# Optimization experiments

Hardware: AMD Instinct MI355X
Metric: run time of the kernel (lower is better)

## Reference

```python
import jax, jax.numpy as jnp
import numpy as np

B, N, F_IN = 8, 4096, 100  # F_IN = num_traj * classification_steps
D = 64                     # node_dim
OUT = 1                    # clasf_out_dim


def setup_inputs() -> dict:
    key = jax.random.key(0)
    ks = jax.random.split(key, 12)
    s = lambda fan_in: 1.0 / np.sqrt(fan_in)
    return {
        "x": jax.random.normal(ks[0], (B, N, F_IN), jnp.float32),
        "adj": jax.random.uniform(ks[1], (B, N, N), jnp.float32),
        "mask": jnp.ones((B, N), jnp.float32),
        "t": jax.random.uniform(ks[2], (B, 1), jnp.float32),
        # GCNConv layer 0: Linear(F_IN -> D)
        "Wg": jax.random.uniform(ks[3], (F_IN, D), jnp.float32, -s(F_IN), s(F_IN)),
        "bg": jnp.zeros((D,), jnp.float32),
        # time_mlp: Linear(1 -> D)
        "Wt": jax.random.uniform(ks[4], (1, D), jnp.float32, -1.0, 1.0),
        "bt": jnp.zeros((D,), jnp.float32),
        # classifier MLP: (2D -> D) -> (D -> D) -> (D -> OUT)
        "W0": jax.random.uniform(ks[5], (2 * D, D), jnp.float32, -s(2 * D), s(2 * D)),
        "b0": jnp.zeros((D,), jnp.float32),
        "W1": jax.random.uniform(ks[6], (D, D), jnp.float32, -s(D), s(D)),
        "b1": jnp.zeros((D,), jnp.float32),
        "W2": jax.random.uniform(ks[7], (D, OUT), jnp.float32, -s(D), s(D)),
        "b2": jnp.zeros((OUT,), jnp.float32),
    }


def reference(x, adj, mask, t, Wg, bg, Wt, bt, W0, b0, W1, b1, W2, b2):
    # GCNConv: linear transform then dense neighbor aggregation, ReLU.
    # (dropout is identity in eval mode)
    h = jnp.einsum("bnf,fd->bnd", x, Wg) + bg          # [B, N, D]
    h = jax.nn.relu(jnp.einsum("bnm,bmd->bnd", adj, h))  # aggregate over neighbors
    # Masked average node pooling
    m = mask[..., None]                                  # [B, N, 1]
    pooled = (h * m).sum(axis=1) / jnp.maximum(mask.sum(axis=1, keepdims=True), 1.0)  # [B, D]
    # time_mlp: Linear(1 -> D)
    te = t @ Wt + bt                                     # [B, D]
    z = jnp.concatenate([pooled, te], axis=1)            # [B, 2D]
    z = jax.nn.relu(z @ W0 + b0)
    z = jax.nn.relu(z @ W1 + b1)
    return jax.nn.sigmoid(z @ W2 + b2)                   # [B, OUT]
```

## Files before the change

kernel.cpp:

```cpp
#include <hip/hip_runtime.h>
#include <hip/hip_bf16.h>
#include <math.h>

#define BB 8
#define NN 4096
#define FF 100
#define DD 64
#define BK 64
#define RT 128

typedef __bf16 bf16x8 __attribute__((ext_vector_type(8)));
typedef float f32x4 __attribute__((ext_vector_type(4)));

__device__ __forceinline__ void gload16(const void* g, void* l) {
    __builtin_amdgcn_global_load_lds(
        (const __attribute__((address_space(1))) unsigned int*)g,
        (__attribute__((address_space(3))) unsigned int*)l, 16, 0, 0);
}
__device__ __forceinline__ void gload16nt(const void* g, void* l) {
    __builtin_amdgcn_global_load_lds(
        (const __attribute__((address_space(1))) unsigned int*)g,
        (__attribute__((address_space(3))) unsigned int*)l, 16, 0, 2);
}

__global__ __launch_bounds__(256) void kernA(
    const float* __restrict__ x, const float* __restrict__ Wg,
    const float* __restrict__ bg, __bf16* __restrict__ hT,
    float* __restrict__ pooled)
{
    __shared__ float lds[64][65];
    int tid = threadIdx.x;
    int g = blockIdx.x * 256 + tid;
    if (g < BB * DD) pooled[g] = 0.0f;

    int b  = blockIdx.x >> 6;
    int m0 = (blockIdx.x & 63) * 64;
    int d  = tid & 63;
    int mg = tid >> 6;

    float acc[16];
    float bias = bg[d];
    #pragma unroll
    for (int j = 0; j < 16; ++j) acc[j] = bias;

    const float* xbase = x + ((size_t)b * NN + m0 + mg * 16) * FF;
    for (int f4 = 0; f4 < FF / 4; ++f4) {
        float wg0 = Wg[(f4 * 4 + 0) * DD + d];
        float wg1 = Wg[(f4 * 4 + 1) * DD + d];
        float wg2 = Wg[(f4 * 4 + 2) * DD + d];
        float wg3 = Wg[(f4 * 4 + 3) * DD + d];
        #pragma unroll
        for (int j = 0; j < 16; ++j) {
            float4 xv = *reinterpret_cast<const float4*>(xbase + j * FF + f4 * 4);
            acc[j] += xv.x * wg0 + xv.y * wg1 + xv.z * wg2 + xv.w * wg3;
        }
    }
    #pragma unroll
    for (int j = 0; j < 16; ++j) lds[mg * 16 + j][d] = acc[j];
    __syncthreads();

    int lane = tid & 63;
    int dg   = tid >> 6;
    size_t obase = ((size_t)b * DD + dg * 16) * NN + m0 + lane;
    #pragma unroll
    for (int j = 0; j < 16; ++j)
        hT[obase + (size_t)j * NN] = (__bf16)lds[lane][dg * 16 + j];
}

__global__ __launch_bounds__(512) void kernB(
    const float* __restrict__ adj, const __bf16* __restrict__ hT,
    const float* __restrict__ mask, float* __restrict__ pooled)
{
    __shared__ float  aL[3][RT * BK];
    __shared__ __bf16 hL[3][DD * BK];

    int l   = blockIdx.x;
    int bb  = l & 7;
    int n0  = (l >> 3) * RT;
    int tid = threadIdx.x;
    int w    = tid >> 6;
    int lane = tid & 63;
    int l15  = lane & 15;
    int kg   = lane >> 4;
    int rowL = w * 16 + l15;
    int rsw  = rowL & 15;
    int dsw  = l15 & 7;

    f32x4 acc[4];
    #pragma unroll
    for (int c = 0; c < 4; ++c) acc[c] = (f32x4){0.f, 0.f, 0.f, 0.f};

    const float*  adjB = adj + ((size_t)bb * NN + n0) * NN;
    const __bf16* hTB  = hT + (size_t)bb * DD * NN;

    auto stage = [&](int buf, int k0) {
        #pragma unroll
        for (int i = 0; i < 4; ++i) {
            int p    = i * 512 + tid;
            int row  = p >> 4;
            int slot = p & 15;
            int ss   = slot ^ (row & 15);
            const float* gp = adjB + (size_t)row * NN + k0 + ss * 4;
            gload16nt(gp, (char*)(&aL[buf][0]) + (size_t)p * 16);
        }
        {
            int p    = tid;
            int d    = p >> 3;
            int slot = p & 7;
            int ss   = slot ^ (d & 7);
            const __bf16* gp = hTB + (size_t)d * NN + k0 + ss * 8;
            gload16(gp, (char*)(&hL[buf][0]) + (size_t)p * 16);
        }
    };

    const int NSTEP = NN / BK;
    stage(0, 0);
    stage(1, BK);

    for (int step = 0; step < NSTEP; ++step) {
        if (step < NSTEP - 1) {
            asm volatile("s_waitcnt vmcnt(5) lgkmcnt(0)" ::: "memory");
        } else {
            asm volatile("s_waitcnt vmcnt(0) lgkmcnt(0)" ::: "memory");
        }
        __builtin_amdgcn_s_barrier();
        if (step + 2 < NSTEP) stage((step + 2) % 3, (step + 2) * BK);

        int cur = step % 3;
        const float*  aB = &aL[cur][rowL * BK];
        const __bf16* hB = &hL[cur][0];
        #pragma unroll
        for (int kk = 0; kk < 2; ++kk) {
            int s0 = kk * 8 + kg * 2;
            f32x4 alo = *(const f32x4*)(aB + ((s0    ) ^ rsw) * 4);
            f32x4 ahi = *(const f32x4*)(aB + ((s0 + 1) ^ rsw) * 4);
            bf16x8 af;
            af[0] = (__bf16)alo[0]; af[1] = (__bf16)alo[1];
            af[2] = (__bf16)alo[2]; af[3] = (__bf16)alo[3];
            af[4] = (__bf16)ahi[0]; af[5] = (__bf16)ahi[1];
            af[6] = (__bf16)ahi[2]; af[7] = (__bf16)ahi[3];
            int slB = (kk * 4 + kg) ^ dsw;
            #pragma unroll
            for (int c = 0; c < 4; ++c) {
                const __bf16* bp = hB + (c * 16 + l15) * BK + slB * 8;
                acc[c] = __builtin_amdgcn_mfma_f32_16x16x32_bf16(
                    af, *(const bf16x8*)bp, acc[c], 0, 0, 0);
            }
        }
    }

    float mk[4];
    int growbase = n0 + w * 16 + kg * 4;
    #pragma unroll
    for (int j = 0; j < 4; ++j) mk[j] = mask[bb * NN + growbase + j];
    #pragma unroll
    for (int c = 0; c < 4; ++c) {
        float s = 0.f;
        #pragma unroll
        for (int j = 0; j < 4; ++j) s += fmaxf(acc[c][j], 0.f) * mk[j];
        s += __shfl_xor(s, 16);
        s += __shfl_xor(s, 32);
        if (lane < 16)
            atomicAdd(&pooled[bb * DD + c * 16 + lane], s);
    }
}

__global__ __launch_bounds__(512) void kernC(
    const float* __restrict__ mask, const float* __restrict__ t_in,
    const float* __restrict__ Wt, const float* __restrict__ bt,
    const float* __restrict__ W0, const float* __restrict__ b0,
    const float* __restrict__ W1, const float* __restrict__ b1,
    const float* __restrict__ W2, const float* __restrict__ b2,
    const float* __restrict__ pooled, float* __restrict__ out)
{
    __shared__ float msum[BB];
    __shared__ float zs[BB][2 * DD];
    __shared__ float z1s[BB][DD];
    __shared__ float z2s[BB][DD];

    int tid  = threadIdx.x;
    int b    = tid >> 6;
    int lane = tid & 63;

    float s = 0.f;
    for (int i = lane; i < NN; i += 64) s += mask[b * NN + i];
    s += __shfl_xor(s, 32); s += __shfl_xor(s, 16);
    s += __shfl_xor(s, 8);  s += __shfl_xor(s, 4);
    s += __shfl_xor(s, 2);  s += __shfl_xor(s, 1);
    if (lane == 0) msum[b] = s;
    __syncthreads();

    float ms  = fmaxf(msum[b], 1.0f);
    float pv  = pooled[b * DD + lane] / ms;
    float tev = t_in[b] * Wt[lane] + bt[lane];
    zs[b][lane]      = pv;
    zs[b][DD + lane] = tev;
    __syncthreads();

    float a = b0[lane];
    for (int f = 0; f < 2 * DD; ++f) a += zs[b][f] * W0[f * DD + lane];
    z1s[b][lane] = fmaxf(a, 0.f);
    __syncthreads();

    a = b1[lane];
    for (int f = 0; f < DD; ++f) a += z1s[b][f] * W1[f * DD + lane];
    z2s[b][lane] = fmaxf(a, 0.f);
    __syncthreads();

    if (lane == 0) {
        float o = b2[0];
        for (int f = 0; f < DD; ++f) o += z2s[b][f] * W2[f];
        out[b] = 1.f / (1.f + expf(-o));
    }
}

extern "C" void kernel_launch(void* const* d_in, const int* in_sizes, int n_in,
                              void* d_out, int out_size, void* d_ws, size_t ws_size,
                              hipStream_t stream)
{
    const float* x    = (const float*)d_in[0];
    const float* adj  = (const float*)d_in[1];
    const float* mask = (const float*)d_in[2];
    const float* t    = (const float*)d_in[3];
    const float* Wg   = (const float*)d_in[4];
    const float* bg   = (const float*)d_in[5];
    const float* Wt   = (const float*)d_in[6];
    const float* bt   = (const float*)d_in[7];
    const float* W0   = (const float*)d_in[8];
    const float* b0   = (const float*)d_in[9];
    const float* W1   = (const float*)d_in[10];
    const float* b1   = (const float*)d_in[11];
    const float* W2   = (const float*)d_in[12];
    const float* b2   = (const float*)d_in[13];
    float* out = (float*)d_out;

    __bf16* hT    = (__bf16*)d_ws;
    float* pooled = (float*)((char*)d_ws + (size_t)BB * DD * NN * 2);

    kernA<<<BB * NN / 64, 256, 0, stream>>>(x, Wg, bg, hT, pooled);
    kernB<<<BB * NN / RT, 512, 0, stream>>>(adj, hT, mask, pooled);
    kernC<<<1, 512, 0, stream>>>(mask, t, Wt, bt, W0, b0, W1, b1, W2, b2,
                                 pooled, out);
}
```

Measured before the change: 172.9 us.

## Replace direct global-to-LDS loads with register-staged double buffering in kernB

The adj/hT tile loads in the aggregation kernel no longer use global_load_lds async copies into a triple-buffered LDS ring. Each thread now loads the next-next tile into registers, writes the next tile from registers into a double-buffered LDS array after computing, then barriers once per step. This cuts LDS use, which may raise occupancy, and makes the pipeline simpler. In exchange it adds VGPR pressure and explicit LDS write instructions, and it drops the non-temporal hint on the adj stream.

Result: slower. 290.7 us (+68.2%).

```diff
diff --git a/kernel.cpp b/kernel.cpp
--- a/kernel.cpp
+++ b/kernel.cpp
@@ -12,17 +12,6 @@
 typedef __bf16 bf16x8 __attribute__((ext_vector_type(8)));
 typedef float f32x4 __attribute__((ext_vector_type(4)));
 
-__device__ __forceinline__ void gload16(const void* g, void* l) {
-    __builtin_amdgcn_global_load_lds(
-        (const __attribute__((address_space(1))) unsigned int*)g,
-        (__attribute__((address_space(3))) unsigned int*)l, 16, 0, 0);
-}
-__device__ __forceinline__ void gload16nt(const void* g, void* l) {
-    __builtin_amdgcn_global_load_lds(
-        (const __attribute__((address_space(1))) unsigned int*)g,
-        (__attribute__((address_space(3))) unsigned int*)l, 16, 0, 2);
-}
-
 __global__ __launch_bounds__(256) void kernA(
     const float* __restrict__ x, const float* __restrict__ Wg,
     const float* __restrict__ bg, __bf16* __restrict__ hT,
@@ -71,8 +60,8 @@
     const float* __restrict__ adj, const __bf16* __restrict__ hT,
     const float* __restrict__ mask, float* __restrict__ pooled)
 {
-    __shared__ float  aL[3][RT * BK];
-    __shared__ __bf16 hL[3][DD * BK];
+    __shared__ float  aL[2][RT * BK];
+    __shared__ __bf16 hL[2][DD * BK];
 
     int l   = blockIdx.x;
     int bb  = l & 7;
@@ -93,40 +82,49 @@
     const float*  adjB = adj + ((size_t)bb * NN + n0) * NN;
     const __bf16* hTB  = hT + (size_t)bb * DD * NN;
 
-    auto stage = [&](int buf, int k0) {
+    const float* srcA[4];
+    #pragma unroll
+    for (int i = 0; i < 4; ++i) {
+        int p    = i * 512 + tid;
+        int row  = p >> 4;
+        int slot = p & 15;
+        int ss   = slot ^ (row & 15);
+        srcA[i]  = adjB + (size_t)row * NN + ss * 4;
+    }
+    const __bf16* srcH;
+    {
+        int p    = tid;
+        int d    = p >> 3;
+        int slot = p & 7;
+        int ss   = slot ^ (d & 7);
+        srcH     = hTB + (size_t)d * NN + ss * 8;
+    }
+
+    float4 rg[5];
+    auto load_tile = [&](int k0) {
+        #pragma unroll
+        for (int i = 0; i < 4; ++i)
+            rg[i] = *reinterpret_cast<const float4*>(srcA[i] + k0);
+        rg[4] = *reinterpret_cast<const float4*>(srcH + k0);
+    };
+    auto write_tile = [&](int buf) {
         #pragma unroll
         for (int i = 0; i < 4; ++i) {
-            int p    = i * 512 + tid;
-            int row  = p >> 4;
-            int slot = p & 15;
-            int ss   = slot ^ (row & 15);
-            const float* gp = adjB + (size_t)row * NN + k0 + ss * 4;
-            gload16nt(gp, (char*)(&aL[buf][0]) + (size_t)p * 16);
-        }
-        {
-            int p    = tid;
-            int d    = p >> 3;
-            int slot = p & 7;
-            int ss   = slot ^ (d & 7);
-            const __bf16* gp = hTB + (size_t)d * NN + k0 + ss * 8;
-            gload16(gp, (char*)(&hL[buf][0]) + (size_t)p * 16);
-        }
+            int p = i * 512 + tid;
+            *reinterpret_cast<float4*>((char*)(&aL[buf][0]) + (size_t)p * 16) = rg[i];
+        }
+        *reinterpret_cast<float4*>((char*)(&hL[buf][0]) + (size_t)tid * 16) = rg[4];
     };
 
     const int NSTEP = NN / BK;
-    stage(0, 0);
-    stage(1, BK);
+    load_tile(0);
+    write_tile(0);
+    load_tile(BK);
+    __syncthreads();
 
     for (int step = 0; step < NSTEP; ++step) {
-        if (step < NSTEP - 1) {
-            asm volatile("s_waitcnt vmcnt(5) lgkmcnt(0)" ::: "memory");
-        } else {
-            asm volatile("s_waitcnt vmcnt(0) lgkmcnt(0)" ::: "memory");
-        }
-        __builtin_amdgcn_s_barrier();
-        if (step + 2 < NSTEP) stage((step + 2) % 3, (step + 2) * BK);
-
-        int cur = step % 3;
+        int cur = step & 1;
+
         const float*  aB = &aL[cur][rowL * BK];
         const __bf16* hB = &hL[cur][0];
         #pragma unroll
@@ -147,6 +145,13 @@
                     af, *(const bf16x8*)bp, acc[c], 0, 0, 0);
             }
         }
+
+        if (step + 1 < NSTEP) {
+            write_tile(cur ^ 1);
+            if (step + 2 < NSTEP) load_tile((step + 2) * BK);
+        }
+        asm volatile("s_waitcnt lgkmcnt(0)" ::: "memory");
+        __builtin_amdgcn_s_barrier();
     }
 
     float mk[4];
```

## Compute node linear transform with bf16 MFMA and change adj load cache policy

Applied to the files above, without the earlier changes.

kernA's x@Wg projection moves from scalar FP32 FMAs to bf16 MFMA 16x16x32 instructions. Wg is transposed into LDS as bf16 and the K dimension is zero-padded from 100 to 128. Separately, the adj tile loads in kernB switch their cache-policy bits from 2 to 18 (a different non-temporal/scope hint). The MFMA path adds bf16 rounding of x and Wg, plus per-block LDS setup that reloads Wg.

Result: faster. 153.6 us (-11.1%).

```diff
diff --git a/kernel.cpp b/kernel.cpp
--- a/kernel.cpp
+++ b/kernel.cpp
@@ -17,10 +17,10 @@
         (const __attribute__((address_space(1))) unsigned int*)g,
         (__attribute__((address_space(3))) unsigned int*)l, 16, 0, 0);
 }
-__device__ __forceinline__ void gload16nt(const void* g, void* l) {
+__device__ __forceinline__ void gload16sc(const void* g, void* l) {
     __builtin_amdgcn_global_load_lds(
         (const __attribute__((address_space(1))) unsigned int*)g,
-        (__attribute__((address_space(3))) unsigned int*)l, 16, 0, 2);
+        (__attribute__((address_space(3))) unsigned int*)l, 16, 0, 18);
 }
 
 __global__ __launch_bounds__(256) void kernA(
@@ -28,39 +28,73 @@
     const float* __restrict__ bg, __bf16* __restrict__ hT,
     float* __restrict__ pooled)
 {
-    __shared__ float lds[64][65];
+    __shared__ __bf16 wgT[DD][136];
+    __shared__ float  lds[64][65];
+
     int tid = threadIdx.x;
     int g = blockIdx.x * 256 + tid;
     if (g < BB * DD) pooled[g] = 0.0f;
 
     int b  = blockIdx.x >> 6;
     int m0 = (blockIdx.x & 63) * 64;
-    int d  = tid & 63;
-    int mg = tid >> 6;
-
-    float acc[16];
-    float bias = bg[d];
-    #pragma unroll
-    for (int j = 0; j < 16; ++j) acc[j] = bias;
-
-    const float* xbase = x + ((size_t)b * NN + m0 + mg * 16) * FF;
-    for (int f4 = 0; f4 < FF / 4; ++f4) {
-        float wg0 = Wg[(f4 * 4 + 0) * DD + d];
-        float wg1 = Wg[(f4 * 4 + 1) * DD + d];
-        float wg2 = Wg[(f4 * 4 + 2) * DD + d];
-        float wg3 = Wg[(f4 * 4 + 3) * DD + d];
-        #pragma unroll
-        for (int j = 0; j < 16; ++j) {
-            float4 xv = *reinterpret_cast<const float4*>(xbase + j * FF + f4 * 4);
-            acc[j] += xv.x * wg0 + xv.y * wg1 + xv.z * wg2 + xv.w * wg3;
-        }
-    }
-    #pragma unroll
-    for (int j = 0; j < 16; ++j) lds[mg * 16 + j][d] = acc[j];
-    __syncthreads();
-
     int lane = tid & 63;
-    int dg   = tid >> 6;
+    int w    = tid >> 6;
+    int l15  = lane & 15;
+    int kg   = lane >> 4;
+
+    for (int i = tid; i < DD * 136; i += 256)
+        wgT[i / 136][i % 136] = (__bf16)0.0f;
+    __syncthreads();
+    for (int i = tid; i < FF * DD; i += 256) {
+        int k = i >> 6, d = i & 63;
+        wgT[d][k] = (__bf16)Wg[i];
+    }
+    __syncthreads();
+
+    f32x4 acc[4];
+    #pragma unroll
+    for (int c = 0; c < 4; ++c) acc[c] = (f32x4){0.f, 0.f, 0.f, 0.f};
+
+    int m = m0 + w * 16 + l15;
+    const float* xrow = x + ((size_t)b * NN + m) * FF;
+
+    #pragma unroll
+    for (int kc = 0; kc < 4; ++kc) {
+        bf16x8 af;
+        if (kc < 3) {
+            float4 xa = *reinterpret_cast<const float4*>(xrow + kc * 32 + kg * 8);
+            float4 xb = *reinterpret_cast<const float4*>(xrow + kc * 32 + kg * 8 + 4);
+            af[0] = (__bf16)xa.x; af[1] = (__bf16)xa.y;
+            af[2] = (__bf16)xa.z; af[3] = (__bf16)xa.w;
+            af[4] = (__bf16)xb.x; af[5] = (__bf16)xb.y;
+            af[6] = (__bf16)xb.z; af[7] = (__bf16)xb.w;
+        } else {
+            float4 xa = (kg == 0)
+                ? *reinterpret_cast<const float4*>(xrow + 96)
+                : (float4){0.f, 0.f, 0.f, 0.f};
+            af[0] = (__bf16)xa.x; af[1] = (__bf16)xa.y;
+            af[2] = (__bf16)xa.z; af[3] = (__bf16)xa.w;
+            af[4] = (__bf16)0.f;  af[5] = (__bf16)0.f;
+            af[6] = (__bf16)0.f;  af[7] = (__bf16)0.f;
+        }
+        #pragma unroll
+        for (int c = 0; c < 4; ++c) {
+            bf16x8 bv = *reinterpret_cast<const bf16x8*>(
+                &wgT[c * 16 + l15][kc * 32 + kg * 8]);
+            acc[c] = __builtin_amdgcn_mfma_f32_16x16x32_bf16(af, bv, acc[c], 0, 0, 0);
+        }
+    }
+
+    #pragma unroll
+    for (int c = 0; c < 4; ++c) {
+        float bias = bg[c * 16 + l15];
+        #pragma unroll
+        for (int j = 0; j < 4; ++j)
+            lds[w * 16 + kg * 4 + j][c * 16 + l15] = acc[c][j] + bias;
+    }
+    __syncthreads();
+
+    int dg = tid >> 6;
     size_t obase = ((size_t)b * DD + dg * 16) * NN + m0 + lane;
     #pragma unroll
     for (int j = 0; j < 16; ++j)
@@ -101,7 +135,7 @@
             int slot = p & 15;
             int ss   = slot ^ (row & 15);
             const float* gp = adjB + (size_t)row * NN + k0 + ss * 4;
-            gload16nt(gp, (char*)(&aL[buf][0]) + (size_t)p * 16);
+            gload16sc(gp, (char*)(&aL[buf][0]) + (size_t)p * 16);
         }
         {
             int p    = tid;
```
